# Optimization experiments

Hardware: AMD Instinct MI355X
Metric: run time of the kernel (lower is better)

## Reference

```python
import jax, jax.numpy as jnp
import numpy as np

P_LEN, Q_LEN, BATCH, D = 1024, 128, 64, 256


def setup_inputs() -> dict:
    key = jax.random.key(0)
    ks = jax.random.split(key, 9)
    sc = 1.0 / np.sqrt(D)
    return {
        "p_data": jax.random.normal(ks[0], (P_LEN, BATCH, D), jnp.float32),
        "q_data": jax.random.normal(ks[1], (Q_LEN, BATCH, D), jnp.float32),
        "v0": jax.random.normal(ks[2], (BATCH, D), jnp.float32),
        "Wpu": jax.random.normal(ks[3], (D, D), jnp.float32) * sc,
        "Wqu": jax.random.normal(ks[4], (D, D), jnp.float32) * sc,
        "Wpv": jax.random.normal(ks[5], (D, D), jnp.float32) * sc,
        "W_ih": jax.random.normal(ks[6], (4 * D, D), jnp.float32) * sc,
        "W_hh": jax.random.normal(ks[7], (4 * D, D), jnp.float32) * sc,
        "b_ih": jnp.zeros((4 * D,), jnp.float32),
        "b_hh": jnp.zeros((4 * D,), jnp.float32),
    }


def reference(p_data, q_data, v0, Wpu, Wqu, Wpv, W_ih, W_hh, b_ih, b_hh):
    # Precompute Wqu @ u_j for all question positions once: (Q, B, D)
    qW = jnp.einsum('qbd,ed->qbe', q_data, Wqu)

    def step(v, ut):
        # v: (B, D) current match state; ut: (B, D) passage word at step t
        base = ut @ Wpu.T + v @ Wpv.T                         # (B, D)
        # s_j = v . (Wqu u_j + Wpu u_t + Wpv v)   -> (Q, B)
        s = jnp.einsum('qbd,bd->qb', qW, v) + jnp.einsum('bd,bd->b', base, v)[None, :]
        # linear normalization over question positions (source uses sum, not softmax)
        a = s / jnp.sum(s, axis=0, keepdims=True)             # (Q, B)
        c_ctx = jnp.einsum('qb,qbd->bd', a, q_data)           # (B, D)
        # LSTM cell: input v, hidden h = u_t, cell = c_ctx (as in source lstm(v, (ut, c)))
        gates = v @ W_ih.T + b_ih + ut @ W_hh.T + b_hh        # (B, 4D)
        i, f, g, o = jnp.split(gates, 4, axis=-1)
        c_new = jax.nn.sigmoid(f) * c_ctx + jax.nn.sigmoid(i) * jnp.tanh(g)
        h_new = jax.nn.sigmoid(o) * jnp.tanh(c_new)
        return h_new, None

    v, _ = jax.lax.scan(step, v0, p_data)
    return v
```

## Files before the change

kernel.cpp:

```cpp
#include <hip/hip_runtime.h>

#define T_LEN 1024
#define B_N   64
#define D_N   256
#define Q_N   128
#define WCOLS 2560
#define GROW  1344
#define NT    256
#define NGRP  16
#define GB    4
#define GWGS  16
#define FSTRIDE 32
#define VP    260
#define VPS   264

typedef __attribute__((ext_vector_type(8))) short short8;
typedef __attribute__((ext_vector_type(4))) float floatx4;

#define MFMA16(A, B, C) __builtin_amdgcn_mfma_f32_16x16x32_bf16((A), (B), (C), 0, 0, 0)

__device__ __forceinline__ float fsigmoid(float x) { return 1.f / (1.f + __expf(-x)); }
__device__ __forceinline__ float ftanh(float x) {
  float ax = fabsf(x);
  float e = __expf(-2.f * ax);
  float r = (1.f - e) / (1.f + e);
  return (x < 0.f) ? -r : r;
}

__device__ __forceinline__ floatx4 ld4_sc(const float* a) {
  floatx4 r;
  asm volatile("global_load_dwordx4 %0, %1, off sc0 sc1" : "=v"(r) : "v"(a) : "memory");
  return r;
}
__device__ __forceinline__ float ld1_sc(const float* a) {
  float r;
  asm volatile("global_load_dword %0, %1, off sc0 sc1" : "=v"(r) : "v"(a) : "memory");
  return r;
}
__device__ __forceinline__ void st1_sc(float* a, float v) {
  asm volatile("global_store_dword %0, %1, off sc0 sc1" :: "v"(a), "v"(v) : "memory");
}
__device__ __forceinline__ void vm_drain() { asm volatile("s_waitcnt vmcnt(0)" ::: "memory"); }
#define TIE(x) asm volatile("" : "+v"(x))

struct Split3 { short8 h, m, l; };
__device__ __forceinline__ Split3 split8(const float* x) {
  union U { unsigned u[4]; short8 s; } H, M, L;
#pragma unroll
  for (int i = 0; i < 4; ++i) {
    float x0 = x[2 * i], x1 = x[2 * i + 1];
    unsigned h0 = __float_as_uint(x0) & 0xffff0000u;
    unsigned h1 = __float_as_uint(x1) & 0xffff0000u;
    float r0 = x0 - __uint_as_float(h0);
    float r1 = x1 - __uint_as_float(h1);
    unsigned m0 = __float_as_uint(r0) & 0xffff0000u;
    unsigned m1 = __float_as_uint(r1) & 0xffff0000u;
    float s0 = r0 - __uint_as_float(m0);
    float s1 = r1 - __uint_as_float(m1);
    H.u[i] = (h0 >> 16) | h1;
    M.u[i] = (m0 >> 16) | m1;
    L.u[i] = (__float_as_uint(s0) >> 16) | (__float_as_uint(s1) & 0xffff0000u);
  }
  Split3 r; r.h = H.s; r.m = M.s; r.l = L.s; return r;
}

__device__ __forceinline__ floatx4 mfma5(floatx4 acc, const Split3& A, short8 Bh, short8 Bm) {
  acc = MFMA16(A.l, Bh, acc);
  acc = MFMA16(A.m, Bm, acc);
  acc = MFMA16(A.m, Bh, acc);
  acc = MFMA16(A.h, Bm, acc);
  acc = MFMA16(A.h, Bh, acc);
  return acc;
}

__global__ void prep_kernel(const float* __restrict__ Wpu, const float* __restrict__ Wqu,
                            const float* __restrict__ Wpv, const float* __restrict__ Wih,
                            const float* __restrict__ Whh,
                            unsigned short* __restrict__ Wh, unsigned short* __restrict__ Wm,
                            float* __restrict__ WquT, unsigned* __restrict__ flags) {
  int idx = blockIdx.x * 256 + threadIdx.x;
  const int total = WCOLS * 256;
  if (idx < total) {
    int n = idx >> 8, k = idx & 255;
    float w;
    if      (n < 256)  w = Wpu[k * 256 + n];
    else if (n < 512)  w = Wpv[k * 256 + (n - 256)];
    else if (n < 1536) w = Wih[(n - 512) * 256 + k];
    else               w = Whh[(n - 1536) * 256 + k];
    unsigned hb = __float_as_uint(w) & 0xffff0000u;
    float r1 = w - __uint_as_float(hb);
    Wh[idx] = (unsigned short)(hb >> 16);
    Wm[idx] = (unsigned short)((__float_as_uint(r1) & 0xffff0000u) >> 16);
  } else if (idx < total + 65536) {
    int i = idx - total, n = i >> 8, k = i & 255;
    WquT[n * 256 + k] = Wqu[k * 256 + n];
  } else if (idx < total + 65536 + 8192) {
    flags[idx - total - 65536] = 0u;
  }
}

__global__ void prep_qz(const float* __restrict__ q, const float* __restrict__ WquT,
                        float* __restrict__ qsout, float* __restrict__ zbout) {
  __shared__ float qsh[256];
  const int b = blockIdx.x, tid = threadIdx.x;
  float s = 0.f;
  for (int j = 0; j < Q_N; ++j) s += q[((size_t)j * B_N + b) * D_N + tid];
  qsout[b * 256 + tid] = s;
  qsh[tid] = s;
  __syncthreads();
  float z = 0.f;
  for (int n = 0; n < 256; ++n) z += WquT[n * 256 + tid] * qsh[n];
  zbout[b * 256 + tid] = z;
}

__global__ void prep_K(const float* __restrict__ q, const float* __restrict__ WquT,
                       unsigned short* __restrict__ KbH, unsigned short* __restrict__ KbM) {
  extern __shared__ float qb[];
  const int b = blockIdx.x >> 2, ic = blockIdx.x & 3, tid = threadIdx.x;
  for (int j = 0; j < Q_N; ++j)
    qb[j * 257 + tid] = q[((size_t)j * B_N + b) * D_N + tid];
  __syncthreads();
  float Kacc[64];
#pragma unroll
  for (int i = 0; i < 64; ++i) Kacc[i] = 0.f;
  const int i0 = ic * 64;
  for (int qc = 0; qc < 16; ++qc) {
    float Pq[8];
#pragma unroll
    for (int qq = 0; qq < 8; ++qq) Pq[qq] = 0.f;
    for (int n = 0; n < 256; ++n) {
      float wv = WquT[n * 256 + tid];
#pragma unroll
      for (int qq = 0; qq < 8; ++qq) Pq[qq] += qb[(qc * 8 + qq) * 257 + n] * wv;
    }
#pragma unroll
    for (int i = 0; i < 64; ++i) {
      float a = 0.f;
#pragma unroll
      for (int qq = 0; qq < 8; ++qq) a += qb[(qc * 8 + qq) * 257 + i0 + i] * Pq[qq];
      Kacc[i] += a;
    }
  }
#pragma unroll
  for (int i = 0; i < 64; ++i) {
    float x = Kacc[i];
    unsigned hb = __float_as_uint(x) & 0xffff0000u;
    float r1 = x - __uint_as_float(hb);
    size_t o = ((size_t)b * 256 + i0 + i) * 256 + tid;
    KbH[o] = (unsigned short)(hb >> 16);
    KbM[o] = (unsigned short)((__float_as_uint(r1) & 0xffff0000u) >> 16);
  }
}

__device__ __forceinline__ void wait_counter(const unsigned* c, unsigned target) {
  unsigned v = __hip_atomic_load(c, __ATOMIC_RELAXED, __HIP_MEMORY_SCOPE_AGENT);
  while (v < target)
    v = __hip_atomic_load(c, __ATOMIC_RELAXED, __HIP_MEMORY_SCOPE_AGENT);
}

__launch_bounds__(NT, 1)
__global__ void pq_main(const float* __restrict__ p,
                        const float* __restrict__ bih, const float* __restrict__ bhh,
                        const unsigned short* __restrict__ Wh,
                        const unsigned short* __restrict__ Wm,
                        const unsigned short* __restrict__ KbH,
                        const unsigned short* __restrict__ KbM,
                        const float* __restrict__ qs, const float* __restrict__ zb,
                        const float* __restrict__ v0,
                        float* G0, float* G1, unsigned* flags,
                        float* __restrict__ out) {
  __shared__ __align__(16) float vsh[GB * VP];
  __shared__ __align__(16) short vshH[GB * VPS];
  __shared__ __align__(16) short vshM[GB * VPS];
  __shared__ __align__(16) short vshL[GB * VPS];
  __shared__ float bL[1024];
  __shared__ float qsL[GB * 256];
  __shared__ float zL[GB * 256];

  const int tid  = threadIdx.x;
  const int bid  = blockIdx.x;
  const int g    = bid & 15;
  const int m    = bid >> 4;
  const int lane = tid & 63;
  const int widx = tid >> 6;
  const int gw   = m * 4 + widx;
  const int n2   = 512  + gw * 16;
  const int n3   = 1536 + gw * 16;
  const int bmd  = gw >> 4;
  const int ct   = gw & 15;
  const int pt   = gw & 31;
  const int kh   = gw >> 5;
  const int n1   = pt * 16;
  const int row  = lane & 15;
  const int arow = lane & 3;
  const int kb   = lane >> 4;
  const int r0q  = lane >> 4;

  unsigned* cnt = flags + g * FSTRIDE;

  const int nb = lane * 4;
  const int bi = widx;

  for (int i = tid; i < 1024; i += NT) bL[i] = bih[i] + bhh[i];
  for (int i = tid; i < GB * 256; i += NT) {
    int r = i >> 8, c = i & 255;
    qsL[i] = qs[(size_t)(g * GB + r) * 256 + c];
    zL[i]  = zb[(size_t)(g * GB + r) * 256 + c];
    float vv = v0[(size_t)(g * GB + r) * 256 + c];
    vsh[r * VP + c] = vv;
    unsigned uh = __float_as_uint(vv) & 0xffff0000u;
    float r1 = vv - __uint_as_float(uh);
    unsigned um = __float_as_uint(r1) & 0xffff0000u;
    float s = r1 - __uint_as_float(um);
    vshH[r * VPS + c] = (short)(uh >> 16);
    vshM[r * VPS + c] = (short)(um >> 16);
    vshL[r * VPS + c] = (short)(__float_as_uint(s) >> 16);
  }
  __syncthreads();

  short8 Bhg[8], Bmg[8], Bh2[8], Bm2[8], Kh[8], Km[8], Bh1[4], Bm1[4];
#pragma unroll
  for (int ks = 0; ks < 8; ++ks) {
    int ko = ks * 32 + kb * 8;
    int c2 = (n2 + row) * 256 + ko;
    int c3 = (n3 + row) * 256 + ko;
    Bhg[ks] = *(const short8*)&Wh[c2];  Bmg[ks] = *(const short8*)&Wm[c2];
    Bh2[ks] = *(const short8*)&Wh[c3];  Bm2[ks] = *(const short8*)&Wm[c3];
    size_t k0 = ((size_t)(g * GB + bmd) * 256 + ct * 16 + row) * 256 + ko;
    Kh[ks] = *(const short8*)&KbH[k0];  Km[ks] = *(const short8*)&KbM[k0];
  }
#pragma unroll
  for (int ks = 0; ks < 4; ++ks) {
    int kop = (kh * 4 + ks) * 32 + kb * 8;
    int c1 = (n1 + row) * 256 + kop;
    Bh1[ks] = *(const short8*)&Wh[c1];  Bm1[ks] = *(const short8*)&Wm[c1];
  }

  floatx4 acc2 = {0.f, 0.f, 0.f, 0.f};
  float wut[4] = {0.f, 0.f, 0.f, 0.f};
  {
    const float* pb = p + ((size_t)0 * B_N + g * GB) * D_N;
#pragma unroll
    for (int ks = 0; ks < 8; ++ks) {
      float xa[8];
      const float* pr = pb + arow * D_N + ks * 32 + kb * 8;
      *(float4*)&xa[0] = *(const float4*)pr;
      *(float4*)&xa[4] = *(const float4*)(pr + 4);
      Split3 A = split8(xa);
      acc2 = mfma5(acc2, A, Bh2[ks], Bm2[ks]);
    }
    if (n1 < 256 && lane < 16) {
#pragma unroll
      for (int r = 0; r < 4; ++r)
        wut[r] = p[((size_t)0 * B_N + g * GB + r) * D_N + n1 + lane];
    }
  }

  for (int t = 0; t < T_LEN; ++t) {
    float* Gc = (t & 1) ? G1 : G0;

    floatx4 accg = {0.f,0.f,0.f,0.f}, mdac = {0.f,0.f,0.f,0.f}, ac1 = {0.f,0.f,0.f,0.f};
#pragma unroll
    for (int ks = 0; ks < 8; ++ks) {
      int co = ks * 32 + kb * 8;
      Split3 A;
      A.h = *(const short8*)&vshH[arow * VPS + co];
      A.m = *(const short8*)&vshM[arow * VPS + co];
      A.l = *(const short8*)&vshL[arow * VPS + co];
      accg = mfma5(accg, A, Bhg[ks], Bmg[ks]);
      mdac = mfma5(mdac, A, Kh[ks], Km[ks]);
      if ((ks >> 2) == kh) ac1 = mfma5(ac1, A, Bh1[ks & 3], Bm1[ks & 3]);
    }

    if (r0q == 0) {
#pragma unroll
      for (int r = 0; r < 4; ++r)
        st1_sc(&Gc[(size_t)(g * GB + r) * GROW + gw * 16 + row],
               accg[r] + acc2[r]);
    }
    {
      float mdv = (bmd == 0) ? mdac[0] : (bmd == 1) ? mdac[1]
                : (bmd == 2) ? mdac[2] : mdac[3];
      if (r0q == 0)
        st1_sc(&Gc[(size_t)(g * GB + bmd) * GROW + 1024 + ct * 16 + row], mdv);
    }
    {
      float pr4[4];
#pragma unroll
      for (int r = 0; r < 4; ++r) {
        pr4[r] = 0.f;
        if (r0q == 0) {
          float w = (n1 < 256) ? wut[r] : vsh[r * VP + (n1 - 256) + row];
          pr4[r] = ac1[r] * w;
        }
      }
#pragma unroll
      for (int off = 1; off < 16; off <<= 1) {
#pragma unroll
        for (int r = 0; r < 4; ++r) pr4[r] += __shfl_xor(pr4[r], off);
      }
      if (lane == 0) {
#pragma unroll
        for (int r = 0; r < 4; ++r)
          st1_sc(&Gc[(size_t)(g * GB + r) * GROW + 1280 + gw], pr4[r]);
      }
    }
    vm_drain();
    if (lane == 0)
      __hip_atomic_fetch_add(cnt, 1u, __ATOMIC_RELAXED, __HIP_MEMORY_SCOPE_AGENT);

    floatx4 acc2n = {0.f,0.f,0.f,0.f};
    float wutn[4] = {0.f, 0.f, 0.f, 0.f};
    if (t + 1 < T_LEN) {
      const float* pb = p + ((size_t)(t + 1) * B_N + g * GB) * D_N;
#pragma unroll
      for (int ks = 0; ks < 8; ++ks) {
        float xa[8];
        const float* pr = pb + arow * D_N + ks * 32 + kb * 8;
        *(float4*)&xa[0] = *(const float4*)pr;
        *(float4*)&xa[4] = *(const float4*)(pr + 4);
        Split3 A = split8(xa);
        acc2n = mfma5(acc2n, A, Bh2[ks], Bm2[ks]);
      }
      if (n1 < 256 && lane < 16) {
#pragma unroll
        for (int r = 0; r < 4; ++r)
          wutn[r] = p[((size_t)(t + 1) * B_N + g * GB + r) * D_N + n1 + lane];
      }
    }

    wait_counter(cnt, (unsigned)(64 * (t + 1)));

    const float* gr = Gc + (size_t)(g * GB + bi) * GROW;
    floatx4 G0v = ld4_sc(gr + nb);
    floatx4 G1v = ld4_sc(gr + 256 + nb);
    floatx4 G2v = ld4_sc(gr + 512 + nb);
    floatx4 G3v = ld4_sc(gr + 768 + nb);
    floatx4 M4  = ld4_sc(gr + 1024 + nb);
    float part  = ld1_sc(gr + 1280 + lane);
    vm_drain();
    TIE(G0v); TIE(G1v); TIE(G2v); TIE(G3v); TIE(M4); TIE(part);

    floatx4 v4 = *(const floatx4*)&vsh[bi * VP + nb];
    float rz = 0.f;
#pragma unroll
    for (int e = 0; e < 4; ++e) rz += zL[bi * 256 + nb + e] * v4[e];
    float sx = part, sy = rz;
#pragma unroll
    for (int off = 1; off < 64; off <<= 1) {
      sx += __shfl_xor(sx, off);
      sy += __shfl_xor(sy, off);
    }
    float beta = sx;
    float invr = 1.f / (sy + 128.f * beta);

    float h4[4];
#pragma unroll
    for (int e = 0; e < 4; ++e) {
      int n = nb + e;
      float cctx = (M4[e] + beta * qsL[bi * 256 + n]) * invr;
      float cn = fsigmoid(G1v[e] + bL[256 + n]) * cctx
               + fsigmoid(G0v[e] + bL[n]) * ftanh(G2v[e] + bL[512 + n]);
      h4[e] = fsigmoid(G3v[e] + bL[768 + n]) * ftanh(cn);
    }
    *(floatx4*)&vsh[bi * VP + nb] = *(const floatx4*)&h4[0];
    {
      union { unsigned u[2]; short s[4]; } PH, PM, PL;
#pragma unroll
      for (int e = 0; e < 4; ++e) {
        unsigned uh = __float_as_uint(h4[e]) & 0xffff0000u;
        float r1 = h4[e] - __uint_as_float(uh);
        unsigned um = __float_as_uint(r1) & 0xffff0000u;
        float s = r1 - __uint_as_float(um);
        PH.s[e] = (short)(uh >> 16);
        PM.s[e] = (short)(um >> 16);
        PL.s[e] = (short)(__float_as_uint(s) >> 16);
      }
      *(unsigned*)&vshH[bi * VPS + nb]     = PH.u[0];
      *(unsigned*)&vshH[bi * VPS + nb + 2] = PH.u[1];
      *(unsigned*)&vshM[bi * VPS + nb]     = PM.u[0];
      *(unsigned*)&vshM[bi * VPS + nb + 2] = PM.u[1];
      *(unsigned*)&vshL[bi * VPS + nb]     = PL.u[0];
      *(unsigned*)&vshL[bi * VPS + nb + 2] = PL.u[1];
    }
    __syncthreads();
    acc2 = acc2n;
#pragma unroll
    for (int r = 0; r < 4; ++r) wut[r] = wutn[r];
  }

  if (m < GB) out[(size_t)(g * GB + m) * 256 + tid] = vsh[m * VP + tid];
}

extern "C" void kernel_launch(void* const* d_in, const int* in_sizes, int n_in,
                              void* d_out, int out_size, void* d_ws, size_t ws_size,
                              hipStream_t stream) {
  const float* p   = (const float*)d_in[0];
  const float* q   = (const float*)d_in[1];
  const float* v0  = (const float*)d_in[2];
  const float* Wpu = (const float*)d_in[3];
  const float* Wqu = (const float*)d_in[4];
  const float* Wpv = (const float*)d_in[5];
  const float* Wih = (const float*)d_in[6];
  const float* Whh = (const float*)d_in[7];
  const float* bih = (const float*)d_in[8];
  const float* bhh = (const float*)d_in[9];
  float* out = (float*)d_out;

  char* ws = (char*)d_ws;
  unsigned short* Wh  = (unsigned short*)(ws + 0x000000);
  unsigned short* Wm  = (unsigned short*)(ws + 0x140000);
  float*    G0     = (float*)(ws + 0x280000);
  float*    G1     = (float*)(ws + 0x2D4000);
  float*    WquT   = (float*)(ws + 0x2D4000);
  unsigned* flags  = (unsigned*)(ws + 0x328000);
  float*    qs     = (float*)(ws + 0x330000);
  float*    zbv    = (float*)(ws + 0x340000);
  unsigned short* KbH = (unsigned short*)(ws + 0x350000);
  unsigned short* KbM = (unsigned short*)(ws + 0xB50000);
  if (ws_size < 0x1360000u) return;

  const int prep_items = WCOLS * 256 + 65536 + 8192;
  prep_kernel<<<(prep_items + 255) / 256, 256, 0, stream>>>(
      Wpu, Wqu, Wpv, Wih, Whh, Wh, Wm, WquT, flags);

  prep_qz<<<64, 256, 0, stream>>>(q, WquT, qs, zbv);

  const size_t k_smem = 128 * 257 * sizeof(float);
  hipFuncSetAttribute(reinterpret_cast<const void*>(prep_K),
                      hipFuncAttributeMaxDynamicSharedMemorySize, (int)k_smem);
  prep_K<<<256, 256, k_smem, stream>>>(q, WquT, KbH, KbM);

  pq_main<<<NGRP * GWGS, NT, 0, stream>>>(p, bih, bhh, Wh, Wm, KbH, KbM, qs, zbv,
                                          v0, G0, G1, flags, out);
}
```

Before: 7.613 ms.

## Replace contended global atomic counter with per-workgroup flags and LDS aggregation

Each wave used to do a global atomic add on one shared counter per group, and every wave spun on that counter. Now the waves of a workgroup first count arrivals in an LDS counter, and the last wave publishes a per-workgroup step flag on its own 64-byte-spaced slot. Waiters poll the 16 flags in parallel lanes with a wave-wide any. The partial-score array moves to a separate compact buffer, so the G row stride shrinks. This removes atomic contention on one cache line, at the cost of more polling loads and ordering that relies on an LDS atomic plus relaxed stores.

```diff
diff --git a/kernel.cpp b/kernel.cpp
--- a/kernel.cpp
+++ b/kernel.cpp
@@ -5,12 +5,11 @@
 #define D_N   256
 #define Q_N   128
 #define WCOLS 2560
-#define GROW  1344
+#define GROW  1280
 #define NT    256
 #define NGRP  16
 #define GB    4
 #define GWGS  16
-#define FSTRIDE 32
 #define VP    260
 #define VPS   264
 
@@ -94,7 +93,7 @@
   } else if (idx < total + 65536) {
     int i = idx - total, n = i >> 8, k = i & 255;
     WquT[n * 256 + k] = Wqu[k * 256 + n];
-  } else if (idx < total + 65536 + 8192) {
+  } else if (idx < total + 65536 + 4096) {
     flags[idx - total - 65536] = 0u;
   }
 }
@@ -152,10 +151,16 @@
   }
 }
 
-__device__ __forceinline__ void wait_counter(const unsigned* c, unsigned target) {
-  unsigned v = __hip_atomic_load(c, __ATOMIC_RELAXED, __HIP_MEMORY_SCOPE_AGENT);
-  while (v < target)
-    v = __hip_atomic_load(c, __ATOMIC_RELAXED, __HIP_MEMORY_SCOPE_AGENT);
+__device__ __forceinline__ void wait_flags16(const unsigned* f, unsigned val) {
+  const int l = threadIdx.x & 63;
+  const unsigned* fp = f + (l & 15) * 16;
+  unsigned v = val;
+  if (l < 16)
+    v = __hip_atomic_load(fp, __ATOMIC_RELAXED, __HIP_MEMORY_SCOPE_AGENT);
+  while (__any((int)(v < val))) {
+    if (l < 16)
+      v = __hip_atomic_load(fp, __ATOMIC_RELAXED, __HIP_MEMORY_SCOPE_AGENT);
+  }
 }
 
 __launch_bounds__(NT, 1)
@@ -167,8 +172,8 @@
                         const unsigned short* __restrict__ KbM,
                         const float* __restrict__ qs, const float* __restrict__ zb,
                         const float* __restrict__ v0,
-                        float* G0, float* G1, unsigned* flags,
-                        float* __restrict__ out) {
+                        float* G0, float* G1, float* Gp0, float* Gp1,
+                        unsigned* flags, float* __restrict__ out) {
   __shared__ __align__(16) float vsh[GB * VP];
   __shared__ __align__(16) short vshH[GB * VPS];
   __shared__ __align__(16) short vshM[GB * VPS];
@@ -176,6 +181,7 @@
   __shared__ float bL[1024];
   __shared__ float qsL[GB * 256];
   __shared__ float zL[GB * 256];
+  __shared__ unsigned wgc;
 
   const int tid  = threadIdx.x;
   const int bid  = blockIdx.x;
@@ -196,11 +202,12 @@
   const int kb   = lane >> 4;
   const int r0q  = lane >> 4;
 
-  unsigned* cnt = flags + g * FSTRIDE;
+  unsigned* flagsG = flags + g * 256;
 
   const int nb = lane * 4;
   const int bi = widx;
 
+  if (tid == 0) wgc = 0u;
   for (int i = tid; i < 1024; i += NT) bL[i] = bih[i] + bhh[i];
   for (int i = tid; i < GB * 256; i += NT) {
     int r = i >> 8, c = i & 255;
@@ -257,7 +264,8 @@
   }
 
   for (int t = 0; t < T_LEN; ++t) {
-    float* Gc = (t & 1) ? G1 : G0;
+    float* Gc  = (t & 1) ? G1 : G0;
+    float* Gpc = (t & 1) ? Gp1 : Gp0;
 
     floatx4 accg = {0.f,0.f,0.f,0.f}, mdac = {0.f,0.f,0.f,0.f}, ac1 = {0.f,0.f,0.f,0.f};
 #pragma unroll
@@ -302,12 +310,16 @@
       if (lane == 0) {
 #pragma unroll
         for (int r = 0; r < 4; ++r)
-          st1_sc(&Gc[(size_t)(g * GB + r) * GROW + 1280 + gw], pr4[r]);
+          st1_sc(&Gpc[g * 512 + gw * 8 + r], pr4[r]);
       }
     }
     vm_drain();
-    if (lane == 0)
-      __hip_atomic_fetch_add(cnt, 1u, __ATOMIC_RELAXED, __HIP_MEMORY_SCOPE_AGENT);
+    if (lane == 0) {
+      unsigned old = atomicAdd(&wgc, 1u);
+      if (old == (unsigned)(4 * t + 3))
+        __hip_atomic_store(flagsG + m * 16, (unsigned)(t + 1),
+                           __ATOMIC_RELAXED, __HIP_MEMORY_SCOPE_AGENT);
+    }
 
     floatx4 acc2n = {0.f,0.f,0.f,0.f};
     float wutn[4] = {0.f, 0.f, 0.f, 0.f};
@@ -329,7 +341,7 @@
       }
     }
 
-    wait_counter(cnt, (unsigned)(64 * (t + 1)));
+    wait_flags16(flagsG, (unsigned)(t + 1));
 
     const float* gr = Gc + (size_t)(g * GB + bi) * GROW;
     floatx4 G0v = ld4_sc(gr + nb);
@@ -337,7 +349,7 @@
     floatx4 G2v = ld4_sc(gr + 512 + nb);
     floatx4 G3v = ld4_sc(gr + 768 + nb);
     floatx4 M4  = ld4_sc(gr + 1024 + nb);
-    float part  = ld1_sc(gr + 1280 + lane);
+    float part  = ld1_sc(&Gpc[g * 512 + lane * 8 + bi]);
     vm_drain();
     TIE(G0v); TIE(G1v); TIE(G2v); TIE(G3v); TIE(M4); TIE(part);
 
@@ -411,16 +423,18 @@
   unsigned short* Wh  = (unsigned short*)(ws + 0x000000);
   unsigned short* Wm  = (unsigned short*)(ws + 0x140000);
   float*    G0     = (float*)(ws + 0x280000);
-  float*    G1     = (float*)(ws + 0x2D4000);
-  float*    WquT   = (float*)(ws + 0x2D4000);
-  unsigned* flags  = (unsigned*)(ws + 0x328000);
-  float*    qs     = (float*)(ws + 0x330000);
-  float*    zbv    = (float*)(ws + 0x340000);
-  unsigned short* KbH = (unsigned short*)(ws + 0x350000);
-  unsigned short* KbM = (unsigned short*)(ws + 0xB50000);
+  float*    G1     = (float*)(ws + 0x2D0000);
+  float*    WquT   = (float*)(ws + 0x2D0000);
+  float*    Gp0    = (float*)(ws + 0x320000);
+  float*    Gp1    = (float*)(ws + 0x328000);
+  unsigned* flags  = (unsigned*)(ws + 0x330000);
+  float*    qs     = (float*)(ws + 0x334000);
+  float*    zbv    = (float*)(ws + 0x344000);
+  unsigned short* KbH = (unsigned short*)(ws + 0x354000);
+  unsigned short* KbM = (unsigned short*)(ws + 0xB54000);
   if (ws_size < 0x1360000u) return;
 
-  const int prep_items = WCOLS * 256 + 65536 + 8192;
+  const int prep_items = WCOLS * 256 + 65536 + 4096;
   prep_kernel<<<(prep_items + 255) / 256, 256, 0, stream>>>(
       Wpu, Wqu, Wpv, Wih, Whh, Wh, Wm, WquT, flags);
 
@@ -432,5 +446,5 @@
   prep_K<<<256, 256, k_smem, stream>>>(q, WquT, KbH, KbM);
 
   pq_main<<<NGRP * GWGS, NT, 0, stream>>>(p, bih, bhh, Wh, Wm, KbH, KbM, qs, zbv,
-                                          v0, G0, G1, flags, out);
-}
+                                          v0, G0, G1, Gp0, Gp1, flags, out);
+}
```

Measured after the change: 7.886 ms. +3.6%, slower.
